# Kernel optimization log

Measured on AMD Instinct MI355X. Metric: run time of the kernel, lower is better.

## Reference

```python
import jax, jax.numpy as jnp
import numpy as np

NUM_GROUPS = 8   # conv groups and GroupNorm groups (get_safe_groups(256,8)==8)
EPS = 1e-5


def setup_inputs() -> dict:
    key = jax.random.key(0)
    k_x, k_w, k_rw, k_ri, k_g, k_b = jax.random.split(key, 6)
    B, Cin, H, W = 8, 256, 64, 64
    E, Cout, K = 8, 256, 2
    x = jax.random.normal(k_x, (B, Cin, H, W), jnp.float32)
    # grouped conv weight: (E*Cout, Cin//groups, 3, 3)
    conv_w = jax.random.normal(k_w, (E * Cout, Cin // NUM_GROUPS, 3, 3), jnp.float32) * 0.02
    routing_weights = jax.random.uniform(k_rw, (B, K), jnp.float32)
    routing_indices = jax.random.randint(k_ri, (B, K), 0, E)
    gamma = 1.0 + 0.1 * jax.random.normal(k_g, (E, Cout), jnp.float32)
    beta = 0.1 * jax.random.normal(k_b, (E, Cout), jnp.float32)
    return {"x": x, "routing_weights": routing_weights, "routing_indices": routing_indices,
            "top_k": K, "conv_w": conv_w, "gamma": gamma, "beta": beta}


def reference(x, routing_weights, routing_indices, top_k, conv_w, gamma, beta):
    B, Cin, H, W = x.shape
    E, Cout = gamma.shape
    # fused grouped 3x3 conv, padding=1, no bias
    fused = jax.lax.conv_general_dilated(
        x, conv_w, window_strides=(1, 1), padding=((1, 1), (1, 1)),
        dimension_numbers=("NCHW", "OIHW", "NCHW"), feature_group_count=NUM_GROUPS)
    fused = fused.reshape(B, E, Cout, H, W)
    idx = routing_indices.reshape(B, top_k)
    wts = routing_weights.reshape(B, top_k)
    # gather the top_k expert outputs per sample: [B, K, Cout, H, W]
    sel = jnp.take_along_axis(fused, idx[:, :, None, None, None], axis=1)
    # per-expert GroupNorm in fp32 with gamma/beta gathered by expert id
    G = NUM_GROUPS
    xs = sel.astype(jnp.float32).reshape(B, top_k, G, Cout // G, H, W)
    mu = xs.mean(axis=(3, 4, 5), keepdims=True)
    var = xs.var(axis=(3, 4, 5), keepdims=True)
    normed = ((xs - mu) * jax.lax.rsqrt(var + EPS)).reshape(B, top_k, Cout, H, W)
    g = gamma[idx][:, :, :, None, None]   # [B, K, Cout, 1, 1]
    b = beta[idx][:, :, :, None, None]
    normed = (normed * g + b).astype(sel.dtype)
    # SiLU then weighted combine over top_k
    act = normed * jax.nn.sigmoid(normed)
    out = jnp.sum(act * wts[:, :, None, None, None], axis=1)  # [B, Cout, H, W]
    return out
```

## Files before the change

kernel.cpp:

```cpp
#include <hip/hip_runtime.h>

typedef __attribute__((ext_vector_type(8))) short bf8_t;
typedef __attribute__((ext_vector_type(4))) float f4_t;

#define BATCH 8
#define HW    4096
#define COUT  256
#define KTOP  2
#define NPAIR 16
#define NG    8
#define EPSV  1e-5f

#define OFF_CONV  0
#define OFF_XTP   8388608
#define OFF_WTB   (8388608 + 1115136)
#define OFF_STATS (8388608 + 1115136 + 294912)

__device__ __forceinline__ unsigned short f2bf(float f) {
    unsigned u = __builtin_bit_cast(unsigned, f);
    u = (u + 0x7FFFu + ((u >> 16) & 1u)) >> 16;
    return (unsigned short)u;
}
__device__ __forceinline__ float bf2f(unsigned short h) {
    return __builtin_bit_cast(float, (unsigned)h << 16);
}

__global__ void prep_w(const float* __restrict__ w, unsigned short* __restrict__ wTb) {
    int idx = blockIdx.x * 256 + threadIdx.x;
    if (idx >= 8 * 9 * 256 * 32) return;
    int i   = idx & 31;
    int c   = (idx >> 5) & 255;
    int et  = idx >> 13;
    int tap = et % 9;
    int e   = et / 9;
    wTb[idx] = f2bf(w[((size_t)(e * 256 + c) * 32 + i) * 9 + tap]);
}

__global__ void prep_x(const float* __restrict__ x, const int* __restrict__ ridx,
                       unsigned short* __restrict__ xtp) {
    __shared__ float t[32][65];
    const int r   = blockIdx.x;
    const int p   = blockIdx.y;
    const int b   = p >> 1;
    const int e   = ridx[p];
    const int tid = threadIdx.x;
    const bool inter = (r >= 1 && r <= 64);
    if (inter) {
        const float* xb = x + (((size_t)b * 256 + e * 32) * 64 + (r - 1)) * 64;
        for (int f = tid; f < 2048; f += 256)
            t[f >> 6][f & 63] = xb[(size_t)(f >> 6) * 4096 + (f & 63)];
    }
    __syncthreads();
    unsigned short* ob = xtp + ((size_t)p * 66 + r) * 66 * 32;
    for (int f = tid; f < 1056; f += 256) {
        int c = f >> 4, chp = f & 15;
        ushort2 v = make_ushort2(0, 0);
        if (inter && c >= 1 && c <= 64)
            v = make_ushort2(f2bf(t[2 * chp][c - 1]), f2bf(t[2 * chp + 1][c - 1]));
        *(ushort2*)(ob + c * 32 + chp * 2) = v;
    }
}

__launch_bounds__(256, 2)
__global__ void conv_mfma(const unsigned short* __restrict__ xtp,
                          const unsigned short* __restrict__ wTb,
                          const int* __restrict__ ridx,
                          unsigned short* __restrict__ convbuf,
                          float* __restrict__ stats)
{
    __shared__ short xs[4 * 66 * 32];

    const int tid = threadIdx.x;
    const int st  = blockIdx.x;
    const int ct  = blockIdx.y;
    const int p   = blockIdx.z;
    const int e   = ridx[p];

    {
        const unsigned short* g = xtp + ((size_t)p * 66 + st * 2) * 66 * 32;
        for (int f = tid; f < 1056; f += 256)
            *(bf8_t*)&xs[f * 8] = *(const bf8_t*)(g + f * 8);
    }
    __syncthreads();

    const int lane = tid & 63;
    const int l15  = lane & 15;
    const int oct  = lane >> 4;
    const int wave = tid >> 6;
    const int wm   = wave >> 1;
    const int wn   = wave & 1;

    const short* Bbase = xs + wn * 2112 + l15 * 32 + oct * 8;
    const unsigned short* Abase =
        wTb + ((size_t)e * 9 * 256 + ct * 128 + wm * 64 + l15) * 32 + oct * 8;

    f4_t acc[4][4];
    #pragma unroll
    for (int mi = 0; mi < 4; ++mi)
        #pragma unroll
        for (int ni = 0; ni < 4; ++ni)
            acc[mi][ni] = (f4_t){0.f, 0.f, 0.f, 0.f};

    #pragma unroll
    for (int tap = 0; tap < 9; ++tap) {
        const int dy = tap / 3, dx = tap % 3;
        bf8_t af[4], bfr[4];
        #pragma unroll
        for (int mi = 0; mi < 4; ++mi)
            af[mi] = *(const bf8_t*)(Abase + tap * 8192 + mi * 512);
        #pragma unroll
        for (int ni = 0; ni < 4; ++ni)
            bfr[ni] = *(const bf8_t*)(Bbase + dy * 2112 + dx * 32 + ni * 512);
        #pragma unroll
        for (int mi = 0; mi < 4; ++mi)
            #pragma unroll
            for (int ni = 0; ni < 4; ++ni)
                acc[mi][ni] = __builtin_amdgcn_mfma_f32_16x16x32_bf16(
                    af[mi], bfr[ni], acc[mi][ni], 0, 0, 0);
    }

    const size_t cbase  = ((size_t)p * 256 + ct * 128 + wm * 64) * 4096;
    const int    spbase = (st * 2 + wn) * 64;
    float s0 = 0.f, q0 = 0.f, s1 = 0.f, q1 = 0.f;
    #pragma unroll
    for (int mi = 0; mi < 4; ++mi) {
        #pragma unroll
        for (int ni = 0; ni < 4; ++ni) {
            #pragma unroll
            for (int r = 0; r < 4; ++r) {
                float v = acc[mi][ni][r];
                int cout_loc = mi * 16 + oct * 4 + r;
                convbuf[cbase + (size_t)cout_loc * 4096 + spbase + ni * 16 + l15] = f2bf(v);
                if (mi < 2) { s0 += v; q0 = fmaf(v, v, q0); }
                else        { s1 += v; q1 = fmaf(v, v, q1); }
            }
        }
    }
    #pragma unroll
    for (int m = 32; m >= 1; m >>= 1) {
        s0 += __shfl_xor(s0, m); q0 += __shfl_xor(q0, m);
        s1 += __shfl_xor(s1, m); q1 += __shfl_xor(q1, m);
    }
    if (lane == 0) {
        int g0 = ct * 4 + wm * 2;
        atomicAdd(&stats[(p * 8 + g0) * 2 + 0], s0);
        atomicAdd(&stats[(p * 8 + g0) * 2 + 1], q0);
        atomicAdd(&stats[(p * 8 + g0 + 1) * 2 + 0], s1);
        atomicAdd(&stats[(p * 8 + g0 + 1) * 2 + 1], q1);
    }
}

__global__ void finalize_k(const unsigned short* __restrict__ conv,
                           const float* __restrict__ stats,
                           const int* __restrict__ ridx,
                           const float* __restrict__ rw,
                           const float* __restrict__ gamma,
                           const float* __restrict__ beta,
                           float* __restrict__ out)
{
    const int tid = threadIdx.x;
    const int rt  = blockIdx.x;
    const int c   = blockIdx.y;
    const int b   = blockIdx.z;
    const int g   = c >> 5;
    const int sp  = rt * 1024 + tid * 4;

    float r0 = 0.f, r1 = 0.f, r2 = 0.f, r3 = 0.f;
    #pragma unroll
    for (int k = 0; k < KTOP; ++k) {
        int   p  = b * KTOP + k;
        int   e  = ridx[p];
        float wk = rw[p];
        float s  = stats[(p * 8 + g) * 2 + 0];
        float sq = stats[(p * 8 + g) * 2 + 1];
        const float cnt = 1.f / 131072.f;
        float mu  = s * cnt;
        float var = fmaf(-mu, mu, sq * cnt);
        float inv = rsqrtf(var + EPSV);
        float ga  = gamma[e * 256 + c] * inv;
        float be  = fmaf(-mu, ga, beta[e * 256 + c]);
        ushort4 v = *(const ushort4*)&conv[((size_t)p * 256 + c) * 4096 + sp];
        float n0 = fmaf(bf2f(v.x), ga, be);
        float n1 = fmaf(bf2f(v.y), ga, be);
        float n2 = fmaf(bf2f(v.z), ga, be);
        float n3 = fmaf(bf2f(v.w), ga, be);
        r0 = fmaf(wk * n0, 1.f / (1.f + __expf(-n0)), r0);
        r1 = fmaf(wk * n1, 1.f / (1.f + __expf(-n1)), r1);
        r2 = fmaf(wk * n2, 1.f / (1.f + __expf(-n2)), r2);
        r3 = fmaf(wk * n3, 1.f / (1.f + __expf(-n3)), r3);
    }
    *(float4*)&out[((size_t)b * 256 + c) * 4096 + sp] = make_float4(r0, r1, r2, r3);
}

extern "C" void kernel_launch(void* const* d_in, const int* in_sizes, int n_in,
                              void* d_out, int out_size, void* d_ws, size_t ws_size,
                              hipStream_t stream) {
    const float* x      = (const float*)d_in[0];
    const float* rw     = (const float*)d_in[1];
    const int*   ridx   = (const int*)  d_in[2];
    const float* conv_w = (const float*)d_in[4];
    const float* gamma  = (const float*)d_in[5];
    const float* beta   = (const float*)d_in[6];
    float* out = (float*)d_out;

    float* ws = (float*)d_ws;
    unsigned short* convbuf = (unsigned short*)(ws + OFF_CONV);
    unsigned short* xtp     = (unsigned short*)(ws + OFF_XTP);
    unsigned short* wTb     = (unsigned short*)(ws + OFF_WTB);
    float*          stats   = ws + OFF_STATS;

    hipMemsetAsync(stats, 0, NPAIR * NG * 2 * sizeof(float), stream);

    hipLaunchKernelGGL(prep_w, dim3(2304), dim3(256), 0, stream, conv_w, wTb);
    hipLaunchKernelGGL(prep_x, dim3(66, 16), dim3(256), 0, stream, x, ridx, xtp);
    hipLaunchKernelGGL(conv_mfma, dim3(32, 2, 16), dim3(256), 0, stream,
                       xtp, wTb, ridx, convbuf, stats);
    hipLaunchKernelGGL(finalize_k, dim3(4, 256, 8), dim3(256), 0, stream,
                       convbuf, stats, ridx, rw, gamma, beta, out);
}
```

Before: 175.2 us.

## Restructure conv tiling, pad LDS rows, fuse stats reset, coalesce weight prep

```diff
diff --git a/kernel.cpp b/kernel.cpp
--- a/kernel.cpp
+++ b/kernel.cpp
@@ -10,11 +10,12 @@
 #define NPAIR 16
 #define NG    8
 #define EPSV  1e-5f
+#define XSTR  40
 
 #define OFF_CONV  0
 #define OFF_XTP   8388608
-#define OFF_WTB   (8388608 + 1115136)
-#define OFF_STATS (8388608 + 1115136 + 294912)
+#define OFF_WTB   (8388608 + 1393920)
+#define OFF_STATS (8388608 + 1393920 + 294912)
 
 __device__ __forceinline__ unsigned short f2bf(float f) {
     unsigned u = __builtin_bit_cast(unsigned, f);
@@ -25,15 +26,23 @@
     return __builtin_bit_cast(float, (unsigned)h << 16);
 }
 
-__global__ void prep_w(const float* __restrict__ w, unsigned short* __restrict__ wTb) {
-    int idx = blockIdx.x * 256 + threadIdx.x;
-    if (idx >= 8 * 9 * 256 * 32) return;
-    int i   = idx & 31;
-    int c   = (idx >> 5) & 255;
-    int et  = idx >> 13;
-    int tap = et % 9;
-    int e   = et / 9;
-    wTb[idx] = f2bf(w[((size_t)(e * 256 + c) * 32 + i) * 9 + tap]);
+__global__ void prep_w(const float* __restrict__ w, unsigned short* __restrict__ wTb,
+                       float* __restrict__ stats) {
+    __shared__ float ls[32 * 288];
+    const int tid = threadIdx.x;
+    const int e   = blockIdx.x >> 3;
+    const int cb  = (blockIdx.x & 7) * 32;
+    if (blockIdx.x == 0 && tid < NPAIR * NG * 2) stats[tid] = 0.f;
+    const float4* src = (const float4*)(w + (size_t)(e * 256 + cb) * 288);
+    for (int f = tid; f < 2304; f += 256) ((float4*)ls)[f] = src[f];
+    __syncthreads();
+    for (int idx = tid; idx < 9216; idx += 256) {
+        int tap = idx >> 10;
+        int rem = idx & 1023;
+        int cc  = rem >> 5;
+        int i   = rem & 31;
+        wTb[((size_t)(e * 9 + tap) * 256 + cb + cc) * 32 + i] = f2bf(ls[cc * 288 + i * 9 + tap]);
+    }
 }
 
 __global__ void prep_x(const float* __restrict__ x, const int* __restrict__ ridx,
@@ -51,34 +60,33 @@
             t[f >> 6][f & 63] = xb[(size_t)(f >> 6) * 4096 + (f & 63)];
     }
     __syncthreads();
-    unsigned short* ob = xtp + ((size_t)p * 66 + r) * 66 * 32;
+    unsigned short* ob = xtp + ((size_t)p * 66 + r) * (66 * XSTR);
     for (int f = tid; f < 1056; f += 256) {
         int c = f >> 4, chp = f & 15;
         ushort2 v = make_ushort2(0, 0);
         if (inter && c >= 1 && c <= 64)
             v = make_ushort2(f2bf(t[2 * chp][c - 1]), f2bf(t[2 * chp + 1][c - 1]));
-        *(ushort2*)(ob + c * 32 + chp * 2) = v;
-    }
-}
-
-__launch_bounds__(256, 2)
+        *(ushort2*)(ob + c * XSTR + chp * 2) = v;
+    }
+}
+
+__launch_bounds__(512, 4)
 __global__ void conv_mfma(const unsigned short* __restrict__ xtp,
                           const unsigned short* __restrict__ wTb,
                           const int* __restrict__ ridx,
                           unsigned short* __restrict__ convbuf,
                           float* __restrict__ stats)
 {
-    __shared__ short xs[4 * 66 * 32];
+    __shared__ short xs[4 * 66 * XSTR];
 
     const int tid = threadIdx.x;
     const int st  = blockIdx.x;
-    const int ct  = blockIdx.y;
-    const int p   = blockIdx.z;
+    const int p   = blockIdx.y;
     const int e   = ridx[p];
 
     {
-        const unsigned short* g = xtp + ((size_t)p * 66 + st * 2) * 66 * 32;
-        for (int f = tid; f < 1056; f += 256)
+        const unsigned short* g = xtp + ((size_t)p * 66 + st * 2) * (66 * XSTR);
+        for (int f = tid; f < 1320; f += 512)
             *(bf8_t*)&xs[f * 8] = *(const bf8_t*)(g + f * 8);
     }
     __syncthreads();
@@ -87,12 +95,11 @@
     const int l15  = lane & 15;
     const int oct  = lane >> 4;
     const int wave = tid >> 6;
-    const int wm   = wave >> 1;
-    const int wn   = wave & 1;
-
-    const short* Bbase = xs + wn * 2112 + l15 * 32 + oct * 8;
-    const unsigned short* Abase =
-        wTb + ((size_t)e * 9 * 256 + ct * 128 + wm * 64 + l15) * 32 + oct * 8;
+    const int wc   = wave & 3;
+    const int ws   = wave >> 2;
+
+    const short* Ab = xs + (ws * 66 + l15) * XSTR + oct * 8;
+    const unsigned short* Bb = wTb + ((size_t)e * 9 * 256 + wc * 64 + l15) * 32 + oct * 8;
 
     f4_t acc[4][4];
     #pragma unroll
@@ -101,39 +108,46 @@
         for (int ni = 0; ni < 4; ++ni)
             acc[mi][ni] = (f4_t){0.f, 0.f, 0.f, 0.f};
 
+    bf8_t bw[2][4];
+    #pragma unroll
+    for (int ni = 0; ni < 4; ++ni)
+        bw[0][ni] = *(const bf8_t*)(Bb + ni * 512);
+
     #pragma unroll
     for (int tap = 0; tap < 9; ++tap) {
         const int dy = tap / 3, dx = tap % 3;
-        bf8_t af[4], bfr[4];
+        if (tap < 8) {
+            #pragma unroll
+            for (int ni = 0; ni < 4; ++ni)
+                bw[(tap + 1) & 1][ni] = *(const bf8_t*)(Bb + (tap + 1) * 8192 + ni * 512);
+        }
+        bf8_t ax[4];
         #pragma unroll
         for (int mi = 0; mi < 4; ++mi)
-            af[mi] = *(const bf8_t*)(Abase + tap * 8192 + mi * 512);
-        #pragma unroll
-        for (int ni = 0; ni < 4; ++ni)
-            bfr[ni] = *(const bf8_t*)(Bbase + dy * 2112 + dx * 32 + ni * 512);
+            ax[mi] = *(const bf8_t*)(Ab + (dy * 66 + mi * 16 + dx) * XSTR);
         #pragma unroll
         for (int mi = 0; mi < 4; ++mi)
             #pragma unroll
             for (int ni = 0; ni < 4; ++ni)
                 acc[mi][ni] = __builtin_amdgcn_mfma_f32_16x16x32_bf16(
-                    af[mi], bfr[ni], acc[mi][ni], 0, 0, 0);
-    }
-
-    const size_t cbase  = ((size_t)p * 256 + ct * 128 + wm * 64) * 4096;
-    const int    spbase = (st * 2 + wn) * 64;
+                    ax[mi], bw[tap & 1][ni], acc[mi][ni], 0, 0, 0);
+    }
+
+    const int sp0 = st * 128 + ws * 64 + oct * 4;
     float s0 = 0.f, q0 = 0.f, s1 = 0.f, q1 = 0.f;
     #pragma unroll
-    for (int mi = 0; mi < 4; ++mi) {
-        #pragma unroll
-        for (int ni = 0; ni < 4; ++ni) {
-            #pragma unroll
-            for (int r = 0; r < 4; ++r) {
-                float v = acc[mi][ni][r];
-                int cout_loc = mi * 16 + oct * 4 + r;
-                convbuf[cbase + (size_t)cout_loc * 4096 + spbase + ni * 16 + l15] = f2bf(v);
-                if (mi < 2) { s0 += v; q0 = fmaf(v, v, q0); }
-                else        { s1 += v; q1 = fmaf(v, v, q1); }
-            }
+    for (int ni = 0; ni < 4; ++ni) {
+        const size_t crow = ((size_t)p * 256 + wc * 64 + ni * 16 + l15) * 4096;
+        #pragma unroll
+        for (int mi = 0; mi < 4; ++mi) {
+            float a0 = acc[mi][ni][0], a1 = acc[mi][ni][1];
+            float a2 = acc[mi][ni][2], a3 = acc[mi][ni][3];
+            ushort4 pk = make_ushort4(f2bf(a0), f2bf(a1), f2bf(a2), f2bf(a3));
+            *(ushort4*)(convbuf + crow + sp0 + mi * 16) = pk;
+            float sl = a0 + a1 + a2 + a3;
+            float ql = fmaf(a0, a0, fmaf(a1, a1, fmaf(a2, a2, a3 * a3)));
+            if (ni < 2) { s0 += sl; q0 += ql; }
+            else        { s1 += sl; q1 += ql; }
         }
     }
     #pragma unroll
@@ -142,7 +156,7 @@
         s1 += __shfl_xor(s1, m); q1 += __shfl_xor(q1, m);
     }
     if (lane == 0) {
-        int g0 = ct * 4 + wm * 2;
+        int g0 = wc * 2;
         atomicAdd(&stats[(p * 8 + g0) * 2 + 0], s0);
         atomicAdd(&stats[(p * 8 + g0) * 2 + 1], q0);
         atomicAdd(&stats[(p * 8 + g0 + 1) * 2 + 0], s1);
@@ -159,37 +173,46 @@
                            float* __restrict__ out)
 {
     const int tid = threadIdx.x;
-    const int rt  = blockIdx.x;
-    const int c   = blockIdx.y;
-    const int b   = blockIdx.z;
+    const int c   = blockIdx.x;
+    const int b   = blockIdx.y;
     const int g   = c >> 5;
-    const int sp  = rt * 1024 + tid * 4;
-
-    float r0 = 0.f, r1 = 0.f, r2 = 0.f, r3 = 0.f;
+
+    float ga[2], be[2], wk[2];
+    const unsigned short* cb[2];
     #pragma unroll
     for (int k = 0; k < KTOP; ++k) {
-        int   p  = b * KTOP + k;
-        int   e  = ridx[p];
-        float wk = rw[p];
+        int p = b * KTOP + k;
+        int e = ridx[p];
+        wk[k] = rw[p];
         float s  = stats[(p * 8 + g) * 2 + 0];
         float sq = stats[(p * 8 + g) * 2 + 1];
         const float cnt = 1.f / 131072.f;
         float mu  = s * cnt;
         float var = fmaf(-mu, mu, sq * cnt);
         float inv = rsqrtf(var + EPSV);
-        float ga  = gamma[e * 256 + c] * inv;
-        float be  = fmaf(-mu, ga, beta[e * 256 + c]);
-        ushort4 v = *(const ushort4*)&conv[((size_t)p * 256 + c) * 4096 + sp];
-        float n0 = fmaf(bf2f(v.x), ga, be);
-        float n1 = fmaf(bf2f(v.y), ga, be);
-        float n2 = fmaf(bf2f(v.z), ga, be);
-        float n3 = fmaf(bf2f(v.w), ga, be);
-        r0 = fmaf(wk * n0, 1.f / (1.f + __expf(-n0)), r0);
-        r1 = fmaf(wk * n1, 1.f / (1.f + __expf(-n1)), r1);
-        r2 = fmaf(wk * n2, 1.f / (1.f + __expf(-n2)), r2);
-        r3 = fmaf(wk * n3, 1.f / (1.f + __expf(-n3)), r3);
-    }
-    *(float4*)&out[((size_t)b * 256 + c) * 4096 + sp] = make_float4(r0, r1, r2, r3);
+        ga[k] = gamma[e * 256 + c] * inv;
+        be[k] = fmaf(-mu, ga[k], beta[e * 256 + c]);
+        cb[k] = conv + ((size_t)p * 256 + c) * 4096;
+    }
+    float* ob = out + ((size_t)b * 256 + c) * 4096;
+    #pragma unroll
+    for (int j = 0; j < 4; ++j) {
+        int sp = j * 1024 + tid * 4;
+        float r0 = 0.f, r1 = 0.f, r2 = 0.f, r3 = 0.f;
+        #pragma unroll
+        for (int k = 0; k < KTOP; ++k) {
+            ushort4 v = *(const ushort4*)(cb[k] + sp);
+            float n0 = fmaf(bf2f(v.x), ga[k], be[k]);
+            float n1 = fmaf(bf2f(v.y), ga[k], be[k]);
+            float n2 = fmaf(bf2f(v.z), ga[k], be[k]);
+            float n3 = fmaf(bf2f(v.w), ga[k], be[k]);
+            r0 = fmaf(wk[k] * n0, 1.f / (1.f + __expf(-n0)), r0);
+            r1 = fmaf(wk[k] * n1, 1.f / (1.f + __expf(-n1)), r1);
+            r2 = fmaf(wk[k] * n2, 1.f / (1.f + __expf(-n2)), r2);
+            r3 = fmaf(wk[k] * n3, 1.f / (1.f + __expf(-n3)), r3);
+        }
+        *(float4*)(ob + sp) = make_float4(r0, r1, r2, r3);
+    }
 }
 
 extern "C" void kernel_launch(void* const* d_in, const int* in_sizes, int n_in,
@@ -209,12 +232,10 @@
     unsigned short* wTb     = (unsigned short*)(ws + OFF_WTB);
     float*          stats   = ws + OFF_STATS;
 
-    hipMemsetAsync(stats, 0, NPAIR * NG * 2 * sizeof(float), stream);
-
-    hipLaunchKernelGGL(prep_w, dim3(2304), dim3(256), 0, stream, conv_w, wTb);
+    hipLaunchKernelGGL(prep_w, dim3(64), dim3(256), 0, stream, conv_w, wTb, stats);
     hipLaunchKernelGGL(prep_x, dim3(66, 16), dim3(256), 0, stream, x, ridx, xtp);
-    hipLaunchKernelGGL(conv_mfma, dim3(32, 2, 16), dim3(256), 0, stream,
+    hipLaunchKernelGGL(conv_mfma, dim3(32, 16), dim3(512), 0, stream,
                        xtp, wTb, ridx, convbuf, stats);
-    hipLaunchKernelGGL(finalize_k, dim3(4, 256, 8), dim3(256), 0, stream,
+    hipLaunchKernelGGL(finalize_k, dim3(256, 8), dim3(256), 0, stream,
                        convbuf, stats, ridx, rw, gamma, beta, out);
 }
```

After: 162.5 us. 1.08x faster.
